# Kernel tuning notes

Measured on AMD Instinct MI355X. Metric: run time of the kernel, lower is better.

Reference implementation:

```python
import jax, jax.numpy as jnp
import numpy as np
import math

B, T, C = 4, 2048, 1024
N_HEAD = 16


def setup_inputs() -> dict:
    key = jax.random.key(0)
    ks = jax.random.split(key, 5)
    s = 0.02
    return {
        "x": jax.random.normal(ks[0], (B, T, C), jnp.float32),
        "W_attn": jax.random.normal(ks[1], (C, 3 * C), jnp.float32) * s,
        "b_attn": jax.random.normal(ks[2], (3 * C,), jnp.float32) * s,
        "W_proj": jax.random.normal(ks[3], (C, C), jnp.float32) * s,
        "b_proj": jax.random.normal(ks[4], (C,), jnp.float32) * s,
    }


def reference(x, W_attn, b_attn, W_proj, b_proj):
    b, t, c = x.shape
    hd = c // N_HEAD  # head dim
    qkv = x @ W_attn + b_attn                       # [B,T,3C]
    q, k, v = jnp.split(qkv, 3, axis=-1)
    # [B,T,C] -> [B,H,T,hd]
    q = q.reshape(b, t, N_HEAD, hd).transpose(0, 2, 1, 3)
    k = k.reshape(b, t, N_HEAD, hd).transpose(0, 2, 1, 3)
    v = v.reshape(b, t, N_HEAD, hd).transpose(0, 2, 1, 3)
    att = jnp.einsum("bhqd,bhkd->bhqk", q, k) * (1.0 / math.sqrt(hd))
    causal = jnp.tril(jnp.ones((t, t), dtype=bool))
    att = jnp.where(causal, att, -jnp.inf)
    att = jax.nn.softmax(att, axis=-1)              # dropout disabled (eval mode)
    y = jnp.einsum("bhqk,bhkd->bhqd", att, v)       # [B,H,T,hd]
    y = y.transpose(0, 2, 1, 3).reshape(b, t, c)
    out = y @ W_proj + b_proj                       # resid dropout disabled (eval)
    return out
```

## Files before the change

### kernel.cpp

```cpp
#include <hip/hip_runtime.h>

#define B_  4
#define T_  2048
#define C_  1024
#define H_  16
#define D_  64
#define BT_ 8192

typedef __bf16 bf16x8 __attribute__((ext_vector_type(8)));
typedef float  f32x4  __attribute__((ext_vector_type(4)));

#define MFMA(a, b, c) __builtin_amdgcn_mfma_f32_16x16x32_bf16((a), (b), (c), 0, 0, 0)
#define LOG2E 1.4426950408889634f

__device__ __forceinline__ float fexp2(float x) {
#if __has_builtin(__builtin_amdgcn_exp2f)
    return __builtin_amdgcn_exp2f(x);
#else
    return __expf(x * 0.6931471805599453f);
#endif
}

__device__ __forceinline__ unsigned short f2bf(float f) {
    union { float f; unsigned u; } v; v.f = f;
    unsigned r = v.u + 0x7FFFu + ((v.u >> 16) & 1u);
    return (unsigned short)(r >> 16);
}

__device__ __forceinline__ void gll16(const unsigned short* g, unsigned short* l) {
    __builtin_amdgcn_global_load_lds((const __attribute__((address_space(1))) void*)g,
                                     (__attribute__((address_space(3))) void*)l, 16, 0, 0);
}

template <int GPR>
__device__ __forceinline__ void stage16(const unsigned short* grow0, size_t stride_us,
                                        unsigned short* lds, int chunk) {
    const int lane = threadIdx.x & 63;
    const int gidx = chunk * 64 + lane;
    const int row  = gidx / GPR, c = gidx % GPR;
    const int csrc = c ^ (row & (GPR - 1));
    gll16(grow0 + (size_t)row * stride_us + csrc * 8, lds + gidx * 8);
}

__global__ __launch_bounds__(256) void prep_kernel(const float* __restrict__ x,
                                                   unsigned short* __restrict__ xb,
                                                   const float* __restrict__ Wa,
                                                   unsigned short* __restrict__ Wab,
                                                   const float* __restrict__ Wp,
                                                   unsigned short* __restrict__ Wpb) {
    __shared__ float tile[32][33];
    const int bid = blockIdx.x;
    if (bid < 8192) {
        int i = bid * 1024 + threadIdx.x * 4;
        float4 v = *(const float4*)&x[i];
        ushort4 o;
        o.x = f2bf(v.x); o.y = f2bf(v.y); o.z = f2bf(v.z); o.w = f2bf(v.w);
        *(ushort4*)&xb[i] = o;
        return;
    }
    const float* in; unsigned short* out; int N, t;
    if (bid < 11264) { t = bid - 8192;  in = Wa; out = Wab; N = 3072; }
    else             { t = bid - 11264; in = Wp; out = Wpb; N = 1024; }
    const int n0 = (t % (N / 32)) * 32, k0 = (t / (N / 32)) * 32;
    const int tr = threadIdx.x >> 3, tc = (threadIdx.x & 7) * 4;
    float4 v = *(const float4*)&in[(size_t)(k0 + tr) * N + n0 + tc];
    tile[tr][tc + 0] = v.x; tile[tr][tc + 1] = v.y;
    tile[tr][tc + 2] = v.z; tile[tr][tc + 3] = v.w;
    __syncthreads();
    ushort4 o;
    o.x = f2bf(tile[tc + 0][tr]);
    o.y = f2bf(tile[tc + 1][tr]);
    o.z = f2bf(tile[tc + 2][tr]);
    o.w = f2bf(tile[tc + 3][tr]);
    *(ushort4*)&out[(size_t)(n0 + tr) * 1024 + k0 + tc] = o;
}

__global__ __launch_bounds__(256) void transpose_v_kernel(const unsigned short* __restrict__ qkv,
                                                          unsigned short* __restrict__ vT) {
    __shared__ unsigned short tile[64][65];
    const int bh = blockIdx.y;
    const int b = bh >> 4, h = bh & 15;
    const int t0 = blockIdx.x * 64;
    const size_t src = (size_t)b * 2048 * 3072 + 2048 + h * 64;
    const size_t dbase = (size_t)bh * (T_ * D_);
    const int r = threadIdx.x >> 2, c = (threadIdx.x & 3) * 16;
    uint4 a0 = *(const uint4*)&qkv[src + (size_t)(t0 + r) * 3072 + c];
    uint4 a1 = *(const uint4*)&qkv[src + (size_t)(t0 + r) * 3072 + c + 8];
    const unsigned short* ap = (const unsigned short*)&a0;
    #pragma unroll
    for (int i = 0; i < 8; ++i) tile[r][c + i] = ap[i];
    ap = (const unsigned short*)&a1;
    #pragma unroll
    for (int i = 0; i < 8; ++i) tile[r][c + 8 + i] = ap[i];
    __syncthreads();
    unsigned short tmp[16];
    #pragma unroll
    for (int i = 0; i < 16; ++i) tmp[i] = tile[c + i][r];
    *(uint4*)&vT[dbase + (size_t)r * T_ + t0 + c]     = *(uint4*)&tmp[0];
    *(uint4*)&vT[dbase + (size_t)r * T_ + t0 + c + 8] = *(uint4*)&tmp[8];
}

template <int MODE, int VDIRECT>
__global__ __launch_bounds__(256) void gemm_bf16_kernel(
    const unsigned short* __restrict__ A,
    const unsigned short* __restrict__ Bt,
    const float* __restrict__ bias,
    float* __restrict__ outF,
    unsigned short* __restrict__ outB,
    unsigned short* __restrict__ vTout,
    int M, int N, int K)
{
    __shared__ __align__(16) unsigned short smem[(MODE == 0 && VDIRECT) ? 10240 : 8192];
    unsigned short* As = smem;
    unsigned short* Bs = smem + 4096;
    const int tid = threadIdx.x;
    const int wave = tid >> 6, lane = tid & 63;
    const int wr = wave >> 1, wc = wave & 1;
    const int g = lane >> 4, li = lane & 15;
    const int m0 = blockIdx.y * 128, n0 = blockIdx.x * 128;

    f32x4 acc[4][4] = {};

    for (int k0 = 0; k0 < K; k0 += 32) {
        __syncthreads();
        stage16<4>(A  + (size_t)m0 * K + k0, K, As, wave * 2);
        stage16<4>(A  + (size_t)m0 * K + k0, K, As, wave * 2 + 1);
        stage16<4>(Bt + (size_t)n0 * K + k0, K, Bs, wave * 2);
        stage16<4>(Bt + (size_t)n0 * K + k0, K, Bs, wave * 2 + 1);
        __syncthreads();
        bf16x8 af[4], bfr[4];
        #pragma unroll
        for (int mi = 0; mi < 4; ++mi) {
            const int row = wr * 64 + mi * 16 + li;
            af[mi] = *(const bf16x8*)&As[row * 32 + ((g ^ (row & 3)) * 8)];
        }
        #pragma unroll
        for (int ni = 0; ni < 4; ++ni) {
            const int row = wc * 64 + ni * 16 + li;
            bfr[ni] = *(const bf16x8*)&Bs[row * 32 + ((g ^ (row & 3)) * 8)];
        }
        #pragma unroll
        for (int mi = 0; mi < 4; ++mi)
            #pragma unroll
            for (int ni = 0; ni < 4; ++ni)
                acc[mi][ni] = MFMA(af[mi], bfr[ni], acc[mi][ni]);
    }

    float bb[4];
    #pragma unroll
    for (int ni = 0; ni < 4; ++ni) bb[ni] = bias[n0 + wc * 64 + ni * 16 + li];

    if (MODE == 0) {
        __syncthreads();
        if (VDIRECT && n0 >= 2048) {
            const int h = (n0 - 2048 + wc * 64) >> 6;
            const int b = m0 >> 11;
            const int tb = (m0 & 2047) + wr * 64;
            unsigned short* vstg = smem + wave * 2560;
            #pragma unroll
            for (int mp = 0; mp < 2; ++mp) {
                #pragma unroll
                for (int mh = 0; mh < 2; ++mh) {
                    const int mi = mp * 2 + mh;
                    #pragma unroll
                    for (int ni = 0; ni < 4; ++ni)
                        #pragma unroll
                        for (int r = 0; r < 4; ++r)
                            vstg[(ni * 16 + li) * 40 + mh * 16 + g * 4 + r]
                                = f2bf(acc[mi][ni][r] + bb[ni]);
                }
                __builtin_amdgcn_wave_barrier();
                uint4 w0 = *(const uint4*)&vstg[lane * 40];
                uint4 w1 = *(const uint4*)&vstg[lane * 40 + 8];
                uint4 w2 = *(const uint4*)&vstg[lane * 40 + 16];
                uint4 w3 = *(const uint4*)&vstg[lane * 40 + 24];
                unsigned short* dp = vTout
                    + (((size_t)(b * 16 + h) * 64 + lane) * 2048 + tb + mp * 32);
                *(uint4*)dp = w0; *(uint4*)&dp[8] = w1;
                *(uint4*)&dp[16] = w2; *(uint4*)&dp[24] = w3;
                __builtin_amdgcn_wave_barrier();
            }
        } else {
            unsigned short* stg = smem + wave * 1152;
            const float qsc = (n0 < 1024) ? 0.125f * LOG2E : 1.0f;
            const int srow = lane & 15, scp = lane >> 4;
            #pragma unroll
            for (int mi = 0; mi < 4; ++mi) {
                #pragma unroll
                for (int ni = 0; ni < 4; ++ni)
                    #pragma unroll
                    for (int r = 0; r < 4; ++r)
                        stg[(g * 4 + r) * 72 + ni * 16 + li] = f2bf((acc[mi][ni][r] + bb[ni]) * qsc);
                __builtin_amdgcn_wave_barrier();
                uint4 w0 = *(const uint4*)&stg[srow * 72 + scp * 16];
                uint4 w1 = *(const uint4*)&stg[srow * 72 + scp * 16 + 8];
                unsigned short* dst = &outB[(size_t)(m0 + wr * 64 + mi * 16 + srow) * N
                                            + n0 + wc * 64 + scp * 16];
                *(uint4*)dst = w0;
                *(uint4*)&dst[8] = w1;
                __builtin_amdgcn_wave_barrier();
            }
        }
    } else {
        #pragma unroll
        for (int mi = 0; mi < 4; ++mi)
            #pragma unroll
            for (int ni = 0; ni < 4; ++ni) {
                const int col = n0 + wc * 64 + ni * 16 + li;
                #pragma unroll
                for (int r = 0; r < 4; ++r)
                    outF[(size_t)(m0 + wr * 64 + mi * 16 + g * 4 + r) * N + col]
                        = acc[mi][ni][r] + bb[ni];
            }
    }
}


__device__ __forceinline__ void stage_half64(const unsigned short* g0, int ldk,
                                             unsigned short* l0, int half) {
    const int wave = threadIdx.x >> 6, lane = threadIdx.x & 63;
    #pragma unroll
    for (int s = 0; s < 2; ++s) {
        const int h = wave * 2 + s;
        const int rowbase = (h >> 3) * 128 + half * 64 + (h & 7) * 8;
        const int row = rowbase + (lane >> 3);
        const int csrc = (lane & 7) ^ (row & 7);
        gll16(g0 + (size_t)row * ldk + csrc * 8, l0 + rowbase * 64 + lane * 8);
    }
}

#define G2_CLOSE   __builtin_amdgcn_s_barrier()
#define G2_CLOSE6  do { asm volatile("s_waitcnt vmcnt(6)" ::: "memory"); \
                        __builtin_amdgcn_s_barrier(); } while (0)
#define G2_CLOSE0  do { asm volatile("s_waitcnt vmcnt(0)" ::: "memory"); \
                        __builtin_amdgcn_s_barrier(); } while (0)

#define G2_PHASE(ASB, BSB, MP, STAGE_STMT, CLOSE_STMT) do {                      \
    if ((MP) == 0) {                                                             \
        _Pragma("unroll") for (int ni_ = 0; ni_ < 4; ++ni_) {                    \
            bfr[ni_][0] = *(const bf16x8*)&(BSB)[boff[ni_][0]];                  \
            bfr[ni_][1] = *(const bf16x8*)&(BSB)[boff[ni_][1]];                  \
        }                                                                        \
    }                                                                            \
    bf16x8 af00 = *(const bf16x8*)&(ASB)[aoff[2 * (MP)][0]];                     \
    bf16x8 af01 = *(const bf16x8*)&(ASB)[aoff[2 * (MP)][1]];                     \
    bf16x8 af10 = *(const bf16x8*)&(ASB)[aoff[2 * (MP) + 1][0]];                 \
    bf16x8 af11 = *(const bf16x8*)&(ASB)[aoff[2 * (MP) + 1][1]];                 \
    STAGE_STMT;                                                                  \
    __builtin_amdgcn_sched_barrier(0);     \
    __builtin_amdgcn_s_barrier();                                                \
    asm volatile("s_waitcnt lgkmcnt(0)" ::: "memory");                           \
    __builtin_amdgcn_sched_barrier(0);                                           \
    __builtin_amdgcn_s_setprio(1);                                               \
    _Pragma("unroll") for (int ni_ = 0; ni_ < 4; ++ni_) {                        \
        acc[2 * (MP)][ni_]     = MFMA(af00, bfr[ni_][0], acc[2 * (MP)][ni_]);    \
        acc[2 * (MP)][ni_]     = MFMA(af01, bfr[ni_][1], acc[2 * (MP)][ni_]);    \
        acc[2 * (MP) + 1][ni_] = MFMA(af10, bfr[ni_][0], acc[2 * (MP) + 1][ni_]);\
        acc[2 * (MP) + 1][ni_] = MFMA(af11, bfr[ni_][1], acc[2 * (MP) + 1][ni_]);\
    }                                                                            \
    __builtin_amdgcn_s_setprio(0);                                               \
    CLOSE_STMT;                                                                  \
  } while (0)

#define G2_KTILE(ASB, BSB, S1, S2, S3, S4, C4) do {                              \
    bf16x8 bfr[4][2];                                                            \
    G2_PHASE(ASB, BSB, 0, S1, G2_CLOSE);                                         \
    G2_PHASE(ASB, BSB, 1, S2, G2_CLOSE);                                         \
    G2_PHASE(ASB, BSB, 2, S3, G2_CLOSE);                                         \
    G2_PHASE(ASB, BSB, 3, S4, C4);                                               \
  } while (0)

__global__ __launch_bounds__(512, 2) void qkv_gemm256_kernel(
    const unsigned short* __restrict__ A,
    const unsigned short* __restrict__ Bt,
    const float* __restrict__ bias,
    unsigned short* __restrict__ outB,
    unsigned short* __restrict__ vTout)
{
    constexpr int Kc = 1024, Nc = 3072;
    constexpr int NI = (Kc / 64) / 2;
    __shared__ __align__(16) unsigned short smem[65536];

    const int tid = threadIdx.x;
    const int wave = tid >> 6, lane = tid & 63;
    const int wr = wave >> 2, wc = wave & 3;
    const int g = lane >> 4, li = lane & 15;

    int bidx, bidy;
    {
        const int gx = gridDim.x, gy = gridDim.y;
        int b = blockIdx.y * gx + blockIdx.x;
        if ((gy & 7) == 0) {
            const int gy8 = gy >> 3;
            const int k = b >> 3;
            bidy = (b & 7) * gy8 + k / gx;
            bidx = k - (k / gx) * gx;
        } else { bidy = blockIdx.y; bidx = blockIdx.x; }
    }
    const int m0 = bidy * 256, n0 = bidx * 256;

    unsigned short* As0 = smem;
    unsigned short* Bs0 = smem + 16384;
    unsigned short* As1 = smem + 32768;
    unsigned short* Bs1 = smem + 49152;

    const unsigned short* Ag = A  + (size_t)m0 * Kc;
    const unsigned short* Bg = Bt + (size_t)n0 * Kc;

    int aoff[8][2], boff[4][2];
    #pragma unroll
    for (int mi = 0; mi < 8; ++mi) {
        const int R = wr * 128 + mi * 16 + li;
        #pragma unroll
        for (int kk = 0; kk < 2; ++kk)
            aoff[mi][kk] = R * 64 + (((kk * 4 + g) ^ (R & 7)) * 8);
    }
    #pragma unroll
    for (int ni = 0; ni < 4; ++ni) {
        const int R = wc * 64 + ni * 16 + li;
        #pragma unroll
        for (int kk = 0; kk < 2; ++kk)
            boff[ni][kk] = R * 64 + (((kk * 4 + g) ^ (R & 7)) * 8);
    }

    f32x4 acc[8][4] = {};

    stage_half64(Bg,      Kc, Bs0, 0);
    stage_half64(Bg,      Kc, Bs0, 1);
    stage_half64(Ag,      Kc, As0, 0);
    stage_half64(Ag,      Kc, As0, 1);
    stage_half64(Bg + 64, Kc, Bs1, 0);
    stage_half64(Bg + 64, Kc, Bs1, 1);
    stage_half64(Ag + 64, Kc, As1, 0);
    asm volatile("s_waitcnt vmcnt(6)" ::: "memory");
    __builtin_amdgcn_s_barrier();

    #pragma unroll 1
    for (int i = 0; i < NI - 1; ++i) {
        const int kA  = (2 * i + 1) * 64;
        const int kB0 = (2 * i + 2) * 64;
        const int kB1 = (2 * i + 3) * 64;
        G2_KTILE(As0, Bs0,
                 stage_half64(Ag + kA,  Kc, As1, 1),
                 stage_half64(Bg + kB0, Kc, Bs0, 0),
                 stage_half64(Bg + kB0, Kc, Bs0, 1),
                 stage_half64(Ag + kB0, Kc, As0, 0),
                 G2_CLOSE6);
        G2_KTILE(As1, Bs1,
                 stage_half64(Ag + kB0, Kc, As0, 1),
                 stage_half64(Bg + kB1, Kc, Bs1, 0),
                 stage_half64(Bg + kB1, Kc, Bs1, 1),
                 stage_half64(Ag + kB1, Kc, As1, 0),
                 G2_CLOSE6);
    }
    G2_KTILE(As0, Bs0,
             stage_half64(Ag + (Kc - 64), Kc, As1, 1),
             (void)0, (void)0, (void)0,
             G2_CLOSE0);
    G2_KTILE(As1, Bs1, (void)0, (void)0, (void)0, (void)0, G2_CLOSE);

    __syncthreads();

    float bb[4];
    #pragma unroll
    for (int ni = 0; ni < 4; ++ni) bb[ni] = bias[n0 + wc * 64 + ni * 16 + li];

    if (n0 >= 2048) {
        const int h  = ((n0 - 2048) >> 6) + wc;
        const int b  = m0 >> 11;
        const int tb = (m0 & 2047) + wr * 128;
        unsigned short* vstg = smem + wave * 2560;
        #pragma unroll
        for (int mp = 0; mp < 4; ++mp) {
            #pragma unroll
            for (int mh = 0; mh < 2; ++mh) {
                const int mi = mp * 2 + mh;
                #pragma unroll
                for (int ni = 0; ni < 4; ++ni)
                    #pragma unroll
                    for (int r = 0; r < 4; ++r)
                        vstg[(ni * 16 + li) * 40 + mh * 16 + g * 4 + r]
                            = f2bf(acc[mi][ni][r] + bb[ni]);
            }
            __builtin_amdgcn_wave_barrier();
            uint4 w0 = *(const uint4*)&vstg[lane * 40];
            uint4 w1 = *(const uint4*)&vstg[lane * 40 + 8];
            uint4 w2 = *(const uint4*)&vstg[lane * 40 + 16];
            uint4 w3 = *(const uint4*)&vstg[lane * 40 + 24];
            unsigned short* dp = vTout
                + (((size_t)(b * 16 + h) * 64 + lane) * 2048 + tb + mp * 32);
            *(uint4*)dp = w0; *(uint4*)&dp[8] = w1;
            *(uint4*)&dp[16] = w2; *(uint4*)&dp[24] = w3;
            __builtin_amdgcn_wave_barrier();
        }
    } else {
        unsigned short* stg = smem + wave * 1152;
        const float qsc = (n0 < 1024) ? 0.125f * LOG2E : 1.0f;
        const int srow = lane & 15, scp = lane >> 4;
        #pragma unroll
        for (int mi = 0; mi < 8; ++mi) {
            #pragma unroll
            for (int ni = 0; ni < 4; ++ni)
                #pragma unroll
                for (int r = 0; r < 4; ++r)
                    stg[(g * 4 + r) * 72 + ni * 16 + li] = f2bf((acc[mi][ni][r] + bb[ni]) * qsc);
            __builtin_amdgcn_wave_barrier();
            uint4 w0 = *(const uint4*)&stg[srow * 72 + scp * 16];
            uint4 w1 = *(const uint4*)&stg[srow * 72 + scp * 16 + 8];
            unsigned short* dst = &outB[(size_t)(m0 + wr * 128 + mi * 16 + srow) * Nc
                                        + n0 + wc * 64 + scp * 16];
            *(uint4*)dst = w0;
            *(uint4*)&dst[8] = w1;
            __builtin_amdgcn_wave_barrier();
        }
    }
}

__global__ __launch_bounds__(256, 4) void flash_attn_kernel(
    const unsigned short* __restrict__ qkv,
    const unsigned short* __restrict__ vT,
    unsigned short* __restrict__ y)
{
    __shared__ __align__(16) unsigned short Ks[2][64 * 64];
    __shared__ __align__(16) unsigned short Vt[2][64 * 64];
    __shared__ __align__(16) unsigned short Pq[4][16][40];
    const int tid = threadIdx.x;
    const int wv = tid >> 6, lane = tid & 63;
    const int g = lane >> 4, li = lane & 15;
    const int bid = blockIdx.x;
    const int xcd = bid & 7, i = bid >> 3;
    const int bh = xcd * 8 + (i & 7);
    const int p  = i >> 3;
    const int qtA = p, qtB = 31 - p;
    const int b = bh >> 4, h = bh & 15;
    const size_t qrowbase = (size_t)b * 2048 * 3072 + h * 64;
    const size_t vbase = (size_t)bh * (D_ * T_);
    const unsigned short* kbase = qkv + qrowbase + 1024;

    const int rowA = qtA * 64 + wv * 16 + li;
    const int rowB = qtB * 64 + wv * 16 + li;

    bf16x8 aqA[2], aqB[2];
    #pragma unroll
    for (int kc = 0; kc < 2; ++kc) {
        aqA[kc] = *(const bf16x8*)&qkv[qrowbase + (size_t)rowA * 3072 + kc * 32 + g * 8];
        aqB[kc] = *(const bf16x8*)&qkv[qrowbase + (size_t)rowB * 3072 + kc * 32 + g * 8];
    }

    f32x4 oA[4] = {}, oB[4] = {};
    float lA = 0.f, lB = 0.f;
    const float OFS = 8.0f * LOG2E;
    const int nkb = qtB + 1;

    stage16<8>(kbase, 3072, Ks[0], wv * 2);
    stage16<8>(kbase, 3072, Ks[0], wv * 2 + 1);
    stage16<8>(vT + vbase, T_, Vt[0], wv * 2);
    stage16<8>(vT + vbase, T_, Vt[0], wv * 2 + 1);

    for (int kb = 0; kb < nkb; ++kb) {
        const int cur = kb & 1;
        __syncthreads();
        if (kb + 1 < nkb) {
            const int kn = (kb + 1) << 6;
            const int nxt = cur ^ 1;
            stage16<8>(kbase + (size_t)kn * 3072, 3072, Ks[nxt], wv * 2);
            stage16<8>(kbase + (size_t)kn * 3072, 3072, Ks[nxt], wv * 2 + 1);
            stage16<8>(vT + vbase + kn, T_, Vt[nxt], wv * 2);
            stage16<8>(vT + vbase + kn, T_, Vt[nxt], wv * 2 + 1);
        }
        const int k0 = kb << 6;
        const bool doA = (kb <= qtA);
        const unsigned short* ksb = Ks[cur];
        const unsigned short* vtb = Vt[cur];

        #pragma unroll
        for (int half = 0; half < 2; ++half) {
            f32x4 sA[2], sB[2];
            #pragma unroll
            for (int t2 = 0; t2 < 2; ++t2) {
                const int krow = (half * 2 + t2) * 16 + li;
                bf16x8 ka0 = *(const bf16x8*)&ksb[krow * 64 + ((g       ^ (krow & 7)) * 8)];
                bf16x8 ka1 = *(const bf16x8*)&ksb[krow * 64 + (((4 + g) ^ (krow & 7)) * 8)];
                f32x4 z = {};
                z = MFMA(ka0, aqB[0], z);
                sB[t2] = MFMA(ka1, aqB[1], z);
                if (doA) {
                    f32x4 z2 = {};
                    z2 = MFMA(ka0, aqA[0], z2);
                    sA[t2] = MFMA(ka1, aqA[1], z2);
                }
            }
            bf16x8 bpA, bpB;
            {
                #pragma unroll
                for (int t2 = 0; t2 < 2; ++t2) {
                    const int kkb = k0 + (half * 2 + t2) * 16;
                    const bool diag = (kb == qtB);
                    ushort4 pw;
                    #pragma unroll
                    for (int r = 0; r < 4; ++r) {
                        float sv = sB[t2][r];
                        if (diag && (kkb + g * 4 + r > rowB)) sv = -1e30f;
                        float pp = fexp2(sv - OFS);
                        lB += pp;
                        ((unsigned short*)&pw)[r] = f2bf(pp);
                    }
                    *(ushort4*)&Pq[wv][li][t2 * 16 + g * 4] = pw;
                }
                __builtin_amdgcn_wave_barrier();
                bpB = *(const bf16x8*)&Pq[wv][li][g * 8];
                __builtin_amdgcn_wave_barrier();
            }
            if (doA) {
                #pragma unroll
                for (int t2 = 0; t2 < 2; ++t2) {
                    const int kkb = k0 + (half * 2 + t2) * 16;
                    const bool diag = (kb == qtA);
                    ushort4 pw;
                    #pragma unroll
                    for (int r = 0; r < 4; ++r) {
                        float sv = sA[t2][r];
                        if (diag && (kkb + g * 4 + r > rowA)) sv = -1e30f;
                        float pp = fexp2(sv - OFS);
                        lA += pp;
                        ((unsigned short*)&pw)[r] = f2bf(pp);
                    }
                    *(ushort4*)&Pq[wv][li][t2 * 16 + g * 4] = pw;
                }
                __builtin_amdgcn_wave_barrier();
                bpA = *(const bf16x8*)&Pq[wv][li][g * 8];
                __builtin_amdgcn_wave_barrier();
            }
            #pragma unroll
            for (int ot = 0; ot < 4; ++ot) {
                const int vrow = ot * 16 + li;
                bf16x8 av = *(const bf16x8*)&vtb[vrow * 64 + (((half * 4 + g) ^ (vrow & 7)) * 8)];
                oB[ot] = MFMA(av, bpB, oB[ot]);
                if (doA) oA[ot] = MFMA(av, bpA, oA[ot]);
            }
            __builtin_amdgcn_wave_barrier();
        }
    }

    #pragma unroll
    for (int t = 0; t < 2; ++t) {
        float l = t ? lB : lA;
        const f32x4* o = t ? oB : oA;
        l += __shfl_xor(l, 16, 64);
        l += __shfl_xor(l, 32, 64);
        float inv = 1.f / l;
        const int trow = (t ? rowB : rowA);
        const size_t yrow = ((size_t)(b * 2048 + trow)) * 1024 + h * 64;
        #pragma unroll
        for (int ot = 0; ot < 4; ++ot) {
            ushort4 pw;
            #pragma unroll
            for (int r = 0; r < 4; ++r)
                ((unsigned short*)&pw)[r] = f2bf(o[ot][r] * inv);
            *(ushort4*)&y[yrow + ot * 16 + g * 4] = pw;
        }
    }
}

extern "C" void kernel_launch(void* const* d_in, const int* in_sizes, int n_in,
                              void* d_out, int out_size, void* d_ws, size_t ws_size,
                              hipStream_t stream)
{
    const float* x      = (const float*)d_in[0];
    const float* W_attn = (const float*)d_in[1];
    const float* b_attn = (const float*)d_in[2];
    const float* W_proj = (const float*)d_in[3];
    const float* b_proj = (const float*)d_in[4];
    float* out = (float*)d_out;

    char* ws = (char*)d_ws;
    size_t off = 0;
    auto alloc = [&](size_t bytes) -> void* {
        void* p = ws + off;
        off += (bytes + 255) & ~(size_t)255;
        return p;
    };
    unsigned short* xb   = (unsigned short*)alloc((size_t)BT_ * C_ * 2);
    unsigned short* Wab  = (unsigned short*)alloc((size_t)3 * C_ * C_ * 2);
    unsigned short* Wpb  = (unsigned short*)alloc((size_t)C_ * C_ * 2);
    unsigned short* qkvb = (unsigned short*)alloc((size_t)BT_ * 3 * C_ * 2);
    unsigned short* yb   = (unsigned short*)alloc((size_t)BT_ * C_ * 2);
    const size_t vt_bytes = (size_t)BT_ * C_ * 2;
    const bool vdirect = (ws_size >= off + vt_bytes);
    unsigned short* vTb = vdirect ? (unsigned short*)alloc(vt_bytes)
                                  : xb;

    prep_kernel<<<12288, 256, 0, stream>>>(x, xb, W_attn, Wab, W_proj, Wpb);

    if (vdirect) {
        qkv_gemm256_kernel<<<dim3(12, 32), 512, 0, stream>>>(
            xb, Wab, b_attn, qkvb, vTb);
    } else {
        gemm_bf16_kernel<0, 0><<<dim3(24, 64), 256, 0, stream>>>(
            xb, Wab, b_attn, nullptr, qkvb, nullptr, BT_, 3 * C_, C_);
        transpose_v_kernel<<<dim3(T_ / 64, B_ * H_), 256, 0, stream>>>(qkvb, vTb);
    }

    flash_attn_kernel<<<1024, 256, 0, stream>>>(qkvb, vTb, yb);

    gemm_bf16_kernel<1, 0><<<dim3(8, 64), 256, 0, stream>>>(
        yb, Wpb, b_proj, out, nullptr, nullptr, BT_, C_, C_);
}
```

Before: 257.4 us.

## Software-pipeline LDS fragment loads across MFMA phases in QKV GEMM

Restructures the QKV GEMM k-tile loop so A fragments for the next phase are loaded from LDS into alternating register sets while the current phase's MFMAs run, with partial lgkmcnt waits. Global staging is regrouped into two slots instead of four, and per-row LDS offsets are replaced by base offsets plus constant strides. The epilogue staging buffer gets an XOR swizzle to cut LDS bank conflicts. This costs more live registers and changes the order of barriers against in-flight stores, which risks hazards if the wait counts are wrong.

```diff
diff --git a/kernel.cpp b/kernel.cpp
--- a/kernel.cpp
+++ b/kernel.cpp
@@ -235,39 +235,61 @@
 #define G2_CLOSE0  do { asm volatile("s_waitcnt vmcnt(0)" ::: "memory"); \
                         __builtin_amdgcn_s_barrier(); } while (0)
 
-#define G2_PHASE(ASB, BSB, MP, STAGE_STMT, CLOSE_STMT) do {                      \
-    if ((MP) == 0) {                                                             \
-        _Pragma("unroll") for (int ni_ = 0; ni_ < 4; ++ni_) {                    \
-            bfr[ni_][0] = *(const bf16x8*)&(BSB)[boff[ni_][0]];                  \
-            bfr[ni_][1] = *(const bf16x8*)&(BSB)[boff[ni_][1]];                  \
-        }                                                                        \
-    }                                                                            \
-    bf16x8 af00 = *(const bf16x8*)&(ASB)[aoff[2 * (MP)][0]];                     \
-    bf16x8 af01 = *(const bf16x8*)&(ASB)[aoff[2 * (MP)][1]];                     \
-    bf16x8 af10 = *(const bf16x8*)&(ASB)[aoff[2 * (MP) + 1][0]];                 \
-    bf16x8 af11 = *(const bf16x8*)&(ASB)[aoff[2 * (MP) + 1][1]];                 \
-    STAGE_STMT;                                                                  \
-    __builtin_amdgcn_sched_barrier(0);     \
+#define G2_GATE(LG) do {                                                         \
+    __builtin_amdgcn_sched_barrier(0);                                           \
     __builtin_amdgcn_s_barrier();                                                \
-    asm volatile("s_waitcnt lgkmcnt(0)" ::: "memory");                           \
+    asm volatile("s_waitcnt lgkmcnt(" #LG ")" ::: "memory");                     \
     __builtin_amdgcn_sched_barrier(0);                                           \
     __builtin_amdgcn_s_setprio(1);                                               \
-    _Pragma("unroll") for (int ni_ = 0; ni_ < 4; ++ni_) {                        \
-        acc[2 * (MP)][ni_]     = MFMA(af00, bfr[ni_][0], acc[2 * (MP)][ni_]);    \
-        acc[2 * (MP)][ni_]     = MFMA(af01, bfr[ni_][1], acc[2 * (MP)][ni_]);    \
-        acc[2 * (MP) + 1][ni_] = MFMA(af10, bfr[ni_][0], acc[2 * (MP) + 1][ni_]);\
-        acc[2 * (MP) + 1][ni_] = MFMA(af11, bfr[ni_][1], acc[2 * (MP) + 1][ni_]);\
+  } while (0)
+#define G2_END  __builtin_amdgcn_s_setprio(0)
+
+#define G2_MFMA16(MP, A0, A1, A2, A3) do {                                       \
+    _Pragma("unroll") for (int n_ = 0; n_ < 4; ++n_) {                           \
+        acc[2 * (MP)][n_]     = MFMA(A0, bfr[n_][0], acc[2 * (MP)][n_]);         \
+        acc[2 * (MP)][n_]     = MFMA(A1, bfr[n_][1], acc[2 * (MP)][n_]);         \
+        acc[2 * (MP) + 1][n_] = MFMA(A2, bfr[n_][0], acc[2 * (MP) + 1][n_]);     \
+        acc[2 * (MP) + 1][n_] = MFMA(A3, bfr[n_][1], acc[2 * (MP) + 1][n_]);     \
+    } } while (0)
+
+#define G2_KTILE(ASB, BSB, S1, S2, C4) do {                                      \
+    bf16x8 bfr[4][2];                                                            \
+    bf16x8 x0, x1, x2, x3, y0, y1, y2, y3;                                       \
+    x0 = *(const bf16x8*)&(ASB)[ab0];                                            \
+    x1 = *(const bf16x8*)&(ASB)[ab1];                                            \
+    x2 = *(const bf16x8*)&(ASB)[ab0 + 1024];                                     \
+    x3 = *(const bf16x8*)&(ASB)[ab1 + 1024];                                     \
+    _Pragma("unroll") for (int n_ = 0; n_ < 4; ++n_) {                           \
+        bfr[n_][0] = *(const bf16x8*)&(BSB)[bb0 + n_ * 1024];                    \
+        bfr[n_][1] = *(const bf16x8*)&(BSB)[bb1 + n_ * 1024];                    \
     }                                                                            \
-    __builtin_amdgcn_s_setprio(0);                                               \
-    CLOSE_STMT;                                                                  \
-  } while (0)
-
-#define G2_KTILE(ASB, BSB, S1, S2, S3, S4, C4) do {                              \
-    bf16x8 bfr[4][2];                                                            \
-    G2_PHASE(ASB, BSB, 0, S1, G2_CLOSE);                                         \
-    G2_PHASE(ASB, BSB, 1, S2, G2_CLOSE);                                         \
-    G2_PHASE(ASB, BSB, 2, S3, G2_CLOSE);                                         \
-    G2_PHASE(ASB, BSB, 3, S4, C4);                                               \
+    __builtin_amdgcn_sched_barrier(0);        \
+                                                                         \
+    y0 = *(const bf16x8*)&(ASB)[ab0 + 2 * 1024];                                 \
+    y1 = *(const bf16x8*)&(ASB)[ab1 + 2 * 1024];                                 \
+    y2 = *(const bf16x8*)&(ASB)[ab0 + 3 * 1024];                                 \
+    y3 = *(const bf16x8*)&(ASB)[ab1 + 3 * 1024];                                 \
+    S1;                                                                          \
+    G2_GATE(4); G2_MFMA16(0, x0, x1, x2, x3); G2_END;                            \
+    __builtin_amdgcn_s_barrier();                                                \
+                                                                         \
+    x0 = *(const bf16x8*)&(ASB)[ab0 + 4 * 1024];                                 \
+    x1 = *(const bf16x8*)&(ASB)[ab1 + 4 * 1024];                                 \
+    x2 = *(const bf16x8*)&(ASB)[ab0 + 5 * 1024];                                 \
+    x3 = *(const bf16x8*)&(ASB)[ab1 + 5 * 1024];                                 \
+    S2;                                                                          \
+    G2_GATE(4); G2_MFMA16(1, y0, y1, y2, y3); G2_END;                            \
+    __builtin_amdgcn_s_barrier();                                                \
+                                                                         \
+    y0 = *(const bf16x8*)&(ASB)[ab0 + 6 * 1024];                                 \
+    y1 = *(const bf16x8*)&(ASB)[ab1 + 6 * 1024];                                 \
+    y2 = *(const bf16x8*)&(ASB)[ab0 + 7 * 1024];                                 \
+    y3 = *(const bf16x8*)&(ASB)[ab1 + 7 * 1024];                                 \
+    G2_GATE(4); G2_MFMA16(2, x0, x1, x2, x3); G2_END;                            \
+    __builtin_amdgcn_s_barrier();                                                \
+                                                                         \
+    G2_GATE(0); G2_MFMA16(3, y0, y1, y2, y3); G2_END;                            \
+    C4;                                                                          \
   } while (0)
 
 __global__ __launch_bounds__(512, 2) void qkv_gemm256_kernel(
@@ -307,21 +329,10 @@
     const unsigned short* Ag = A  + (size_t)m0 * Kc;
     const unsigned short* Bg = Bt + (size_t)n0 * Kc;
 
-    int aoff[8][2], boff[4][2];
-    #pragma unroll
-    for (int mi = 0; mi < 8; ++mi) {
-        const int R = wr * 128 + mi * 16 + li;
-        #pragma unroll
-        for (int kk = 0; kk < 2; ++kk)
-            aoff[mi][kk] = R * 64 + (((kk * 4 + g) ^ (R & 7)) * 8);
-    }
-    #pragma unroll
-    for (int ni = 0; ni < 4; ++ni) {
-        const int R = wc * 64 + ni * 16 + li;
-        #pragma unroll
-        for (int kk = 0; kk < 2; ++kk)
-            boff[ni][kk] = R * 64 + (((kk * 4 + g) ^ (R & 7)) * 8);
-    }
+    const int ab0 = (wr * 128 + li) * 64 + ((g ^ (li & 7)) * 8);
+    const int ab1 = (wr * 128 + li) * 64 + (((4 + g) ^ (li & 7)) * 8);
+    const int bb0 = (wc * 64 + li) * 64 + ((g ^ (li & 7)) * 8);
+    const int bb1 = (wc * 64 + li) * 64 + (((4 + g) ^ (li & 7)) * 8);
 
     f32x4 acc[8][4] = {};
 
@@ -341,23 +352,23 @@
         const int kB0 = (2 * i + 2) * 64;
         const int kB1 = (2 * i + 3) * 64;
         G2_KTILE(As0, Bs0,
-                 stage_half64(Ag + kA,  Kc, As1, 1),
-                 stage_half64(Bg + kB0, Kc, Bs0, 0),
-                 stage_half64(Bg + kB0, Kc, Bs0, 1),
-                 stage_half64(Ag + kB0, Kc, As0, 0),
+                 stage_half64(Ag + kA, Kc, As1, 1),
+                 (stage_half64(Bg + kB0, Kc, Bs0, 0),
+                  stage_half64(Bg + kB0, Kc, Bs0, 1),
+                  stage_half64(Ag + kB0, Kc, As0, 0)),
                  G2_CLOSE6);
         G2_KTILE(As1, Bs1,
                  stage_half64(Ag + kB0, Kc, As0, 1),
-                 stage_half64(Bg + kB1, Kc, Bs1, 0),
-                 stage_half64(Bg + kB1, Kc, Bs1, 1),
-                 stage_half64(Ag + kB1, Kc, As1, 0),
+                 (stage_half64(Bg + kB1, Kc, Bs1, 0),
+                  stage_half64(Bg + kB1, Kc, Bs1, 1),
+                  stage_half64(Ag + kB1, Kc, As1, 0)),
                  G2_CLOSE6);
     }
     G2_KTILE(As0, Bs0,
              stage_half64(Ag + (Kc - 64), Kc, As1, 1),
-             (void)0, (void)0, (void)0,
+             (void)0,
              G2_CLOSE0);
-    G2_KTILE(As1, Bs1, (void)0, (void)0, (void)0, (void)0, G2_CLOSE);
+    G2_KTILE(As1, Bs1, (void)0, (void)0, G2_CLOSE);
 
     __syncthreads();
 
@@ -403,10 +414,12 @@
             for (int ni = 0; ni < 4; ++ni)
                 #pragma unroll
                 for (int r = 0; r < 4; ++r)
-                    stg[(g * 4 + r) * 72 + ni * 16 + li] = f2bf((acc[mi][ni][r] + bb[ni]) * qsc);
+                    stg[(g * 4 + r) * 72 + ((ni ^ g) * 16) + li]
+                        = f2bf((acc[mi][ni][r] + bb[ni]) * qsc);
             __builtin_amdgcn_wave_barrier();
-            uint4 w0 = *(const uint4*)&stg[srow * 72 + scp * 16];
-            uint4 w1 = *(const uint4*)&stg[srow * 72 + scp * 16 + 8];
+            const int pg = scp ^ (srow >> 2);
+            uint4 w0 = *(const uint4*)&stg[srow * 72 + pg * 16];
+            uint4 w1 = *(const uint4*)&stg[srow * 72 + pg * 16 + 8];
             unsigned short* dst = &outB[(size_t)(m0 + wr * 128 + mi * 16 + srow) * Nc
                                         + n0 + wc * 64 + scp * 16];
             *(uint4*)dst = w0;
```

Result: slower. 268.8 us (+4.4%).

## Single-buffer QKV GEMM LDS with quarter-tile staging to halve shared memory

Applied to the files above, without the earlier changes.

Replaces the double-buffered 128KB LDS pipeline of the QKV GEMM with a single 64KB buffer. A-tile rows are staged in quarter chunks interleaved with the MFMA phases that have finished reading them, and B is reloaded mid-tile, with tuned vmcnt waits per phase. This lowers the LDS footprint, which could allow more resident blocks or simpler scheduling. In exchange it adds more barriers and waits per k-tile and gives loads less time to hide latency.

```diff
diff --git a/kernel.cpp b/kernel.cpp
--- a/kernel.cpp
+++ b/kernel.cpp
@@ -229,23 +229,30 @@
     }
 }
 
+__device__ __forceinline__ void stage_q(const unsigned short* g0, int ldk,
+                                        unsigned short* l0, int q) {
+    const int wave = threadIdx.x >> 6, lane = threadIdx.x & 63;
+    const int rowbase = (wave >> 2) * 128 + q * 32 + (wave & 3) * 8;
+    const int row = rowbase + (lane >> 3);
+    const int csrc = (lane & 7) ^ (row & 7);
+    gll16(g0 + (size_t)row * ldk + csrc * 8, l0 + rowbase * 64 + lane * 8);
+}
+
 #define G2_CLOSE   __builtin_amdgcn_s_barrier()
-#define G2_CLOSE6  do { asm volatile("s_waitcnt vmcnt(6)" ::: "memory"); \
-                        __builtin_amdgcn_s_barrier(); } while (0)
-#define G2_CLOSE0  do { asm volatile("s_waitcnt vmcnt(0)" ::: "memory"); \
-                        __builtin_amdgcn_s_barrier(); } while (0)
-
-#define G2_PHASE(ASB, BSB, MP, STAGE_STMT, CLOSE_STMT) do {                      \
+#define G2_CLOSEN(N) do { asm volatile("s_waitcnt vmcnt(" #N ")" ::: "memory"); \
+                          __builtin_amdgcn_s_barrier(); } while (0)
+
+#define G2_PHASE(MP, STAGE_STMT, CLOSE_STMT) do {                                \
     if ((MP) == 0) {                                                             \
         _Pragma("unroll") for (int ni_ = 0; ni_ < 4; ++ni_) {                    \
-            bfr[ni_][0] = *(const bf16x8*)&(BSB)[boff[ni_][0]];                  \
-            bfr[ni_][1] = *(const bf16x8*)&(BSB)[boff[ni_][1]];                  \
+            bfr[ni_][0] = *(const bf16x8*)&Bs[boff[ni_][0]];                     \
+            bfr[ni_][1] = *(const bf16x8*)&Bs[boff[ni_][1]];                     \
         }                                                                        \
     }                                                                            \
-    bf16x8 af00 = *(const bf16x8*)&(ASB)[aoff[2 * (MP)][0]];                     \
-    bf16x8 af01 = *(const bf16x8*)&(ASB)[aoff[2 * (MP)][1]];                     \
-    bf16x8 af10 = *(const bf16x8*)&(ASB)[aoff[2 * (MP) + 1][0]];                 \
-    bf16x8 af11 = *(const bf16x8*)&(ASB)[aoff[2 * (MP) + 1][1]];                 \
+    bf16x8 af00 = *(const bf16x8*)&As[aoff[2 * (MP)][0]];                        \
+    bf16x8 af01 = *(const bf16x8*)&As[aoff[2 * (MP)][1]];                        \
+    bf16x8 af10 = *(const bf16x8*)&As[aoff[2 * (MP) + 1][0]];                    \
+    bf16x8 af11 = *(const bf16x8*)&As[aoff[2 * (MP) + 1][1]];                    \
     STAGE_STMT;                                                                  \
     __builtin_amdgcn_sched_barrier(0);     \
     __builtin_amdgcn_s_barrier();                                                \
@@ -262,12 +269,12 @@
     CLOSE_STMT;                                                                  \
   } while (0)
 
-#define G2_KTILE(ASB, BSB, S1, S2, S3, S4, C4) do {                              \
+#define G2_KTILE(S1, S2, S3, S4, C1, C2, C3, C4) do {                            \
     bf16x8 bfr[4][2];                                                            \
-    G2_PHASE(ASB, BSB, 0, S1, G2_CLOSE);                                         \
-    G2_PHASE(ASB, BSB, 1, S2, G2_CLOSE);                                         \
-    G2_PHASE(ASB, BSB, 2, S3, G2_CLOSE);                                         \
-    G2_PHASE(ASB, BSB, 3, S4, C4);                                               \
+    G2_PHASE(0, S1, C1);                                                         \
+    G2_PHASE(1, S2, C2);                                                         \
+    G2_PHASE(2, S3, C3);                                                         \
+    G2_PHASE(3, S4, C4);                                                         \
   } while (0)
 
 __global__ __launch_bounds__(512, 2) void qkv_gemm256_kernel(
@@ -278,8 +285,8 @@
     unsigned short* __restrict__ vTout)
 {
     constexpr int Kc = 1024, Nc = 3072;
-    constexpr int NI = (Kc / 64) / 2;
-    __shared__ __align__(16) unsigned short smem[65536];
+    constexpr int NT = Kc / 64;
+    __shared__ __align__(16) unsigned short smem[32768];
 
     const int tid = threadIdx.x;
     const int wave = tid >> 6, lane = tid & 63;
@@ -299,10 +306,8 @@
     }
     const int m0 = bidy * 256, n0 = bidx * 256;
 
-    unsigned short* As0 = smem;
-    unsigned short* Bs0 = smem + 16384;
-    unsigned short* As1 = smem + 32768;
-    unsigned short* Bs1 = smem + 49152;
+    unsigned short* As = smem;
+    unsigned short* Bs = smem + 16384;
 
     const unsigned short* Ag = A  + (size_t)m0 * Kc;
     const unsigned short* Bg = Bt + (size_t)n0 * Kc;
@@ -325,39 +330,32 @@
 
     f32x4 acc[8][4] = {};
 
-    stage_half64(Bg,      Kc, Bs0, 0);
-    stage_half64(Bg,      Kc, Bs0, 1);
-    stage_half64(Ag,      Kc, As0, 0);
-    stage_half64(Ag,      Kc, As0, 1);
-    stage_half64(Bg + 64, Kc, Bs1, 0);
-    stage_half64(Bg + 64, Kc, Bs1, 1);
-    stage_half64(Ag + 64, Kc, As1, 0);
-    asm volatile("s_waitcnt vmcnt(6)" ::: "memory");
+    stage_half64(Bg, Kc, Bs, 0);
+    stage_half64(Bg, Kc, Bs, 1);
+    stage_q(Ag, Kc, As, 0);
+    stage_q(Ag, Kc, As, 1);
+    stage_q(Ag, Kc, As, 2);
+    asm volatile("s_waitcnt vmcnt(0)" ::: "memory");
     __builtin_amdgcn_s_barrier();
 
     #pragma unroll 1
-    for (int i = 0; i < NI - 1; ++i) {
-        const int kA  = (2 * i + 1) * 64;
-        const int kB0 = (2 * i + 2) * 64;
-        const int kB1 = (2 * i + 3) * 64;
-        G2_KTILE(As0, Bs0,
-                 stage_half64(Ag + kA,  Kc, As1, 1),
-                 stage_half64(Bg + kB0, Kc, Bs0, 0),
-                 stage_half64(Bg + kB0, Kc, Bs0, 1),
-                 stage_half64(Ag + kB0, Kc, As0, 0),
-                 G2_CLOSE6);
-        G2_KTILE(As1, Bs1,
-                 stage_half64(Ag + kB0, Kc, As0, 1),
-                 stage_half64(Bg + kB1, Kc, Bs1, 0),
-                 stage_half64(Bg + kB1, Kc, Bs1, 1),
-                 stage_half64(Ag + kB1, Kc, As1, 0),
-                 G2_CLOSE6);
-    }
-    G2_KTILE(As0, Bs0,
-             stage_half64(Ag + (Kc - 64), Kc, As1, 1),
-             (void)0, (void)0, (void)0,
-             G2_CLOSE0);
-    G2_KTILE(As1, Bs1, (void)0, (void)0, (void)0, (void)0, G2_CLOSE);
+    for (int u = 0; u < NT - 1; ++u) {
+        const unsigned short* Au = Ag + u * 64;
+        const unsigned short* An = Au + 64;
+        const unsigned short* Bn = Bg + (u + 1) * 64;
+        G2_KTILE(
+            stage_q(Au, Kc, As, 3),
+            (stage_q(An, Kc, As, 0),
+             stage_half64(Bn, Kc, Bs, 0),
+             stage_half64(Bn, Kc, Bs, 1)),
+            stage_q(An, Kc, As, 1),
+            stage_q(An, Kc, As, 2),
+            G2_CLOSEN(2), G2_CLOSEN(6), G2_CLOSEN(6), G2_CLOSEN(2));
+    }
+    G2_KTILE(
+        stage_q(Ag + (NT - 1) * 64, Kc, As, 3),
+        (void)0, (void)0, (void)0,
+        G2_CLOSEN(2), G2_CLOSEN(1), G2_CLOSEN(0), G2_CLOSE);
 
     __syncthreads();
 
```

Result: no change. 256.6 us (-0.3%).
